# Kernel optimization log

Measured on AMD Instinct MI355X. Metric: run time of the kernel, lower is better.

The kernel has to match this reference:

```python
import jax, jax.numpy as jnp
import numpy as np

N_CHANNELS = 384  # full probe size
N_UNITS = 400     # rows of the sparse log-lik matrix
INT_SENTINEL = np.int32(2**31 - 1)


def setup_inputs() -> dict:
    key = jax.random.key(0)
    k1, k2, k3, k4, k5, k6 = jax.random.split(key, 6)
    n, r, na = 65536, 5, 32
    feats = jax.random.normal(k1, (n, r, na), dtype=jnp.float32)
    # contiguous, duplicate-free channel neighborhood per spike
    starts = jax.random.randint(k2, (n,), 0, N_CHANNELS - na)
    channels = starts[:, None] + jnp.arange(na)  # (n, na) int
    nan_mask = jax.random.uniform(k3, (n, na)) < 0.1
    feats = jnp.where(nan_mask[:, None, :], jnp.nan, feats)
    weights = jax.random.uniform(k4, (n,), dtype=jnp.float32) + 0.01
    # sparse (N_UNITS, n) log-lik matrix in COO, ~10 candidate units per spike
    nnz_per = 10
    nnz = n * nnz_per
    lik_cols = jnp.repeat(jnp.arange(n, dtype=jnp.int32), nnz_per)
    lik_rows = jax.random.randint(k5, (nnz,), 0, N_UNITS, dtype=jnp.int32)
    lik_data = jax.random.normal(k6, (nnz,), dtype=jnp.float32)
    return dict(features=feats, channels=channels, weights=weights,
                lik_rows=lik_rows, lik_cols=lik_cols, lik_data=lik_data)


def reference(features, channels, weights, lik_rows, lik_cols, lik_data):
    n, r, na = features.shape
    C = N_CHANNELS

    # --- to_full_probe: scatter sparse channel features to dense probe ---
    spike_ix = jnp.arange(n)[:, None, None]
    rank_ix = jnp.arange(r)[None, :, None]
    chan_ix = channels[:, None, :]                    # (n, 1, na) -> bcast (n, r, na)
    features_full = jnp.zeros((n, r, C), features.dtype)
    features_full = features_full.at[spike_ix, rank_ix, chan_ix].set(features)

    # finite mask on rank-0 slice, scaled by per-spike weights
    finite = jnp.isfinite(features_full[:, 0, :]).astype(features.dtype)  # (n, C)
    weights_full = finite * weights[:, None]
    features_full = jnp.nan_to_num(features_full)
    count_data = weights_full.sum(0)                  # (C,)
    weights_normalized = weights_full / count_data    # (n, C)

    # fit_mean (prior_type='none'): weighted empirical mean over spikes
    emp_mean = jnp.einsum('nc,nrc->rc', weights_normalized, features_full)  # (r, C)

    # --- sparse_reassign: per-spike-column argmax, sparse zeros = -inf ---
    offset = lik_data.min() - 1.0
    shifted = lik_data - offset                       # strictly positive
    colmax = jax.ops.segment_max(shifted, lik_cols, num_segments=n)
    is_max = shifted == colmax[lik_cols]
    cand = jnp.where(is_max, lik_rows, INT_SENTINEL)
    assign = jax.ops.segment_min(cand, lik_cols, num_segments=n)
    assignments = jnp.where(assign == INT_SENTINEL, -1, assign)  # (n,)

    return emp_mean, assignments
```

## Files before the change

kernel.cpp:

```cpp
#include <hip/hip_runtime.h>
#include <math.h>

#define NCH 384
#define RNK 5
#define NA  32
#define NSTART 384
#define NREP 8
#define CAPR 128
#define CAP (NREP*CAPR)
#define GRID 1536
#define NTILES (NSTART*4)
#define TILE_W 192
#define FLT_BIG 3.402823466e38f

#define WS_CUR   0
#define WS_TOTP  (WS_CUR + NSTART*NREP)
#define WS_MINP  (WS_TOTP + GRID)
#define WS_ORDER (WS_MINP + GRID)
#define WS_TILE  (WS_ORDER + NSTART*CAP*2)
#define WS_WORDS (WS_TILE + NTILES*TILE_W)

__device__ __forceinline__ bool finitef(float v) {
    return fabsf(v) <= FLT_BIG;
}

__global__ __launch_bounds__(256) void k_init(
    const float* __restrict__ lik_data, int nnz,
    unsigned* __restrict__ wsu, float* __restrict__ wsf)
{
    const int tid = threadIdx.x, bid = blockIdx.x;
    const int lane = tid & 63, wave = tid >> 6;
    int i = bid * 256 + tid;
    if (i < NSTART * NREP) wsu[WS_CUR + i] = 0u;

    float m = FLT_BIG;
    const int G = GRID * 256;
    const int n4 = nnz >> 2;
    const float4* d4 = (const float4*)lik_data;
    for (int j = bid * 256 + tid; j < n4; j += G) {
        float4 v = d4[j];
        m = fminf(m, fminf(fminf(v.x, v.y), fminf(v.z, v.w)));
    }
    for (int j = (n4 << 2) + bid * 256 + tid; j < nnz; j += G)
        m = fminf(m, lik_data[j]);

    #pragma unroll
    for (int o = 32; o; o >>= 1) m = fminf(m, __shfl_down(m, o));
    __shared__ float sm[4];
    if (lane == 0) sm[wave] = m;
    __syncthreads();
    if (tid == 0)
        wsf[WS_MINP + bid] = fminf(fminf(sm[0], sm[1]), fminf(sm[2], sm[3]));
}

__global__ __launch_bounds__(256) void k_prep(
    const int* __restrict__ channels, const float* __restrict__ weights,
    int n, unsigned* __restrict__ wsu, float* __restrict__ wsf)
{
    const int tid = threadIdx.x, bid = blockIdx.x;
    const int lane = tid & 63, wave = tid >> 6;
    const int rep = bid & (NREP - 1);
    const int G = GRID * 256;
    uint2* order = (uint2*)(wsu + WS_ORDER);

    float tw = 0.f;
    for (int sp = bid * 256 + tid; sp < n; sp += G) {
        const int st = channels[(size_t)sp * NA];
        const float wv = weights[sp];
        unsigned pos = atomicAdd(&wsu[WS_CUR + st * NREP + rep], 1u);
        if (pos < CAPR)
            order[(size_t)st * CAP + rep * CAPR + pos] =
                make_uint2((unsigned)sp, __float_as_uint(wv));
        tw += wv;
    }

    #pragma unroll
    for (int o = 32; o; o >>= 1) tw += __shfl_down(tw, o);
    __shared__ float st4[4];
    if (lane == 0) st4[wave] = tw;
    __syncthreads();
    if (tid == 0)
        wsf[WS_TOTP + bid] = st4[0] + st4[1] + st4[2] + st4[3];
}

__global__ __launch_bounds__(256) void k_accum(
    const float* __restrict__ feats, const unsigned* __restrict__ wsu,
    float* __restrict__ wsf)
{
    __shared__ float s_tile[TILE_W];
    const int bid = blockIdx.x, tid = threadIdx.x;
    const int b = bid >> 2, tj = bid & 3;
    const int lane = tid & 63, wave = tid >> 6;

    for (int i = tid; i < TILE_W; i += 256) s_tile[i] = 0.f;
    __syncthreads();

    float acc0 = 0.f, acc1 = 0.f, acc2 = 0.f, nanw = 0.f;
    #pragma unroll
    for (int seg = 0; seg < 2; ++seg) {
        const int rep = tj * 2 + seg;
        int cnt = (int)wsu[WS_CUR + b * NREP + rep];
        if (cnt > CAPR) cnt = CAPR;
        const uint2* order =
            (const uint2*)(wsu + WS_ORDER) + (size_t)b * CAP + rep * CAPR;
        uint2 e = make_uint2(0u, 0u);
        if (wave < cnt) e = order[wave];
        for (int k = wave; k < cnt; k += 4) {
            const int spike = (int)e.x;
            const float w = __uint_as_float(e.y);
            const float* f = feats + (size_t)spike * (RNK * NA);
            uint2 ne = make_uint2(0u, 0u);
            if (k + 4 < cnt) ne = order[k + 4];
            const float v0 = f[lane];
            const float v1 = f[lane + 64];
            const float v2 = (lane < 32) ? f[lane + 128] : 0.f;
            const float r0 = __shfl(v0, lane & 31);
            if (finitef(r0)) {
                acc0 += w * (finitef(v0) ? v0 : 0.f);
                acc1 += w * (finitef(v1) ? v1 : 0.f);
                if (lane < 32) acc2 += w * (finitef(v2) ? v2 : 0.f);
            } else if (lane < 32) {
                nanw += w;
            }
            e = ne;
        }
    }

    atomicAdd(&s_tile[lane], acc0);
    atomicAdd(&s_tile[64 + lane], acc1);
    if (lane < 32) {
        atomicAdd(&s_tile[128 + lane], acc2);
        atomicAdd(&s_tile[160 + lane], nanw);
    }
    __syncthreads();

    float* dst = wsf + WS_TILE + (size_t)bid * TILE_W;
    for (int i = tid; i < TILE_W; i += 256) dst[i] = s_tile[i];
}

__global__ __launch_bounds__(256) void k_final(
    const int* __restrict__ lik_rows, const float* __restrict__ lik_data,
    float* __restrict__ wsf, float* __restrict__ out, int n, int per)
{
    const int tid = threadIdx.x, bid = blockIdx.x;
    const int lane = tid & 63, wave = tid >> 6;
    const bool emp_block = (bid * 4 < RNK * NCH);

    float m = FLT_BIG, t = 0.f;
    if (emp_block) {
        for (int i = tid; i < GRID; i += 256) {
            m = fminf(m, wsf[WS_MINP + i]);
            t += wsf[WS_TOTP + i];
        }
    } else {
        for (int i = tid; i < GRID; i += 256)
            m = fminf(m, wsf[WS_MINP + i]);
    }
    #pragma unroll
    for (int o = 32; o; o >>= 1) {
        m = fminf(m, __shfl_down(m, o));
        t += __shfl_down(t, o);
    }
    __shared__ float sm[4], st4[4];
    if (lane == 0) { sm[wave] = m; st4[wave] = t; }
    __syncthreads();
    const float mn  = fminf(fminf(sm[0], sm[1]), fminf(sm[2], sm[3]));
    const float tot = st4[0] + st4[1] + st4[2] + st4[3];

    const float offset = mn - 1.0f;
    const int G = gridDim.x * 256;
    for (int sp = bid * 256 + tid; sp < n; sp += G) {
        const float* d  = lik_data + (size_t)sp * per;
        const int*   rr = lik_rows + (size_t)sp * per;
        float bs = -FLT_BIG;
        int br = 0x7FFFFFFF;
        for (int j = 0; j < per; ++j) {
            float s = d[j] - offset;
            int r = rr[j];
            if (s > bs) { bs = s; br = r; }
            else if (s == bs && r < br) br = r;
        }
        out[RNK * NCH + sp] = (float)br;
    }

    const int wg = bid * 4 + wave;
    if (wg < RNK * NCH) {
        const int c = wg % NCH, r = wg / NCH;
        const int db = lane & 31, half = lane >> 5;
        float s = 0.f, nb = 0.f;
        const int b = c - db;
        if (b >= 0) {
            #pragma unroll
            for (int jj = 0; jj < 2; ++jj) {
                const float* tp =
                    wsf + WS_TILE + ((size_t)b * 4 + jj * 2 + half) * TILE_W;
                s  += tp[r * 32 + db];
                nb += tp[160 + db];
            }
        }
        #pragma unroll
        for (int o = 32; o; o >>= 1) {
            s  += __shfl_down(s, o);
            nb += __shfl_down(nb, o);
        }
        if (lane == 0) out[wg] = s / (tot - nb);
    }
}

#define FB_NUM   0
#define FB_NANW  (RNK*NCH)
#define FB_TOT   (FB_NANW + NCH)
#define FB_MIN   (FB_TOT + 1)
#define FB_WORDS (FB_MIN + 1)

__device__ __forceinline__ unsigned fenc(float f) {
    unsigned u = __float_as_uint(f);
    return (u & 0x80000000u) ? ~u : (u | 0x80000000u);
}
__device__ __forceinline__ float fdec(unsigned u) {
    unsigned b = (u & 0x80000000u) ? (u ^ 0x80000000u) : ~u;
    return __uint_as_float(b);
}
__global__ void fb_init_kernel(unsigned* ws) {
    int i = blockIdx.x * blockDim.x + threadIdx.x;
    if (i < FB_WORDS) ws[i] = (i == FB_MIN) ? 0xFFFFFFFFu : 0u;
}
__global__ __launch_bounds__(256) void fb_accum_kernel(
    const float* feats, const int* channels, const float* weights,
    float* ws, int n)
{
    __shared__ float s_num[RNK * NCH];
    __shared__ float s_nanw[NCH];
    __shared__ float s_total;
    const int tid = threadIdx.x;
    for (int i = tid; i < RNK * NCH; i += 256) s_num[i] = 0.f;
    for (int i = tid; i < NCH; i += 256) s_nanw[i] = 0.f;
    if (tid == 0) s_total = 0.f;
    __syncthreads();
    const int total = n * NA;
    const int stride = gridDim.x * blockDim.x;
    float tw = 0.f;
    for (int idx = blockIdx.x * blockDim.x + tid; idx < total; idx += stride) {
        const int spike = idx >> 5, a = idx & (NA - 1);
        const int ch = channels[idx];
        const float w = weights[spike];
        if (a == 0) tw += w;
        const float* f = feats + (size_t)spike * (RNK * NA) + a;
        const float v0 = f[0];
        if (finitef(v0)) {
            atomicAdd(&s_num[ch], w * v0);
            #pragma unroll
            for (int r = 1; r < RNK; ++r) {
                float v = f[r * NA];
                if (!finitef(v)) v = 0.f;
                atomicAdd(&s_num[r * NCH + ch], w * v);
            }
        } else atomicAdd(&s_nanw[ch], w);
    }
    #pragma unroll
    for (int off = 32; off; off >>= 1) tw += __shfl_down(tw, off);
    if ((tid & 63) == 0) atomicAdd(&s_total, tw);
    __syncthreads();
    for (int i = tid; i < RNK * NCH; i += 256)
        if (s_num[i] != 0.f) atomicAdd(&ws[FB_NUM + i], s_num[i]);
    for (int i = tid; i < NCH; i += 256)
        if (s_nanw[i] != 0.f) atomicAdd(&ws[FB_NANW + i], s_nanw[i]);
    if (tid == 0) atomicAdd(&ws[FB_TOT], s_total);
}
__global__ void fb_min_kernel(const float* data, int nnz, unsigned* minw) {
    float m = FLT_BIG;
    for (int i = blockIdx.x * blockDim.x + threadIdx.x; i < nnz;
         i += gridDim.x * blockDim.x) m = fminf(m, data[i]);
    #pragma unroll
    for (int off = 32; off; off >>= 1) m = fminf(m, __shfl_down(m, off));
    if ((threadIdx.x & 63) == 0) atomicMin(minw, fenc(m));
}
__global__ void fb_finalize_kernel(const float* ws, float* out) {
    int i = blockIdx.x * blockDim.x + threadIdx.x;
    if (i < RNK * NCH) {
        int c = i % NCH;
        float cnt = ws[FB_TOT] - ws[FB_NANW + c];
        out[i] = ws[FB_NUM + i] / cnt;
    }
}
__global__ __launch_bounds__(256) void fb_assign_kernel(
    const int* rows, const float* data, const unsigned* minw,
    float* out, int n, int per)
{
    const int spike = blockIdx.x * 256 + threadIdx.x;
    if (spike >= n) return;
    const float offset = fdec(*minw) - 1.0f;
    const float* d  = data + (size_t)spike * per;
    const int*   rr = rows + (size_t)spike * per;
    float bs = -FLT_BIG;
    int br = 0x7FFFFFFF;
    for (int j = 0; j < per; ++j) {
        float s = d[j] - offset;
        int r = rr[j];
        if (s > bs) { bs = s; br = r; }
        else if (s == bs && r < br) br = r;
    }
    out[RNK * NCH + spike] = (float)br;
}

extern "C" void kernel_launch(void* const* d_in, const int* in_sizes, int n_in,
                              void* d_out, int out_size, void* d_ws, size_t ws_size,
                              hipStream_t stream) {
    const float* feats    = (const float*)d_in[0];
    const int*   channels = (const int*)d_in[1];
    const float* weights  = (const float*)d_in[2];
    const int*   lik_rows = (const int*)d_in[3];
    const float* lik_data = (const float*)d_in[5];

    int n   = in_sizes[2];
    int nnz = in_sizes[3];
    int per = nnz / n;

    float*    out = (float*)d_out;
    unsigned* wsu = (unsigned*)d_ws;
    float*    wsf = (float*)d_ws;

    const size_t req_bytes = (size_t)WS_WORDS * 4;
    const bool cap_ok = (n <= NSTART * NREP * CAPR / 4);

    if (ws_size >= req_bytes && cap_ok) {
        k_init<<<GRID, 256, 0, stream>>>(lik_data, nnz, wsu, wsf);
        k_prep<<<GRID, 256, 0, stream>>>(channels, weights, n, wsu, wsf);
        k_accum<<<NSTART * 4, 256, 0, stream>>>(feats, wsu, wsf);
        k_final<<<GRID, 256, 0, stream>>>(lik_rows, lik_data, wsf, out, n, per);
    } else {
        fb_init_kernel<<<(FB_WORDS + 255) / 256, 256, 0, stream>>>(wsu);
        fb_accum_kernel<<<1024, 256, 0, stream>>>(feats, channels, weights, wsf, n);
        fb_finalize_kernel<<<(RNK * NCH + 255) / 256, 256, 0, stream>>>(wsf, out);
        fb_min_kernel<<<256, 256, 0, stream>>>(lik_data, nnz, wsu + FB_MIN);
        fb_assign_kernel<<<(n + 255) / 256, 256, 0, stream>>>(
            lik_rows, lik_data, wsu + FB_MIN, out, n, per);
    }
}
```

Before: 42.41 us.

## Move sparse argmax assignment into accum kernel as extra blocks

The per-spike argmax reassignment moves out of the final kernel and runs in 256 extra blocks appended to the accumulation launch, so it overlaps with the feature accumulation work. The final kernel then shrinks to only the blocks needed for the empirical mean and no longer reduces the min partials. The intent is to shorten the serial tail after accumulation. In exchange, the assignment blocks now compete for compute units with the accum blocks, and the final kernel's grid size changes.

```diff
diff --git a/kernel.cpp b/kernel.cpp
--- a/kernel.cpp
+++ b/kernel.cpp
@@ -10,6 +10,8 @@
 #define CAP (NREP*CAPR)
 #define GRID 1536
 #define NTILES (NSTART*4)
+#define ASSIGN_GRID 256
+#define EMP_GRID ((RNK*NCH + 3) / 4)
 #define TILE_W 192
 #define FLT_BIG 3.402823466e38f
 
@@ -85,12 +87,44 @@
 
 __global__ __launch_bounds__(256) void k_accum(
     const float* __restrict__ feats, const unsigned* __restrict__ wsu,
-    float* __restrict__ wsf)
+    float* __restrict__ wsf,
+    const int* __restrict__ lik_rows, const float* __restrict__ lik_data,
+    float* __restrict__ out, int n, int per)
 {
     __shared__ float s_tile[TILE_W];
+    __shared__ float sm[4];
     const int bid = blockIdx.x, tid = threadIdx.x;
+    const int lane = tid & 63, wave = tid >> 6;
+
+    if (bid >= NTILES) {
+        const int abid = bid - NTILES;
+        float m = FLT_BIG;
+        for (int i = tid; i < GRID; i += 256) m = fminf(m, wsf[WS_MINP + i]);
+        #pragma unroll
+        for (int o = 32; o; o >>= 1) m = fminf(m, __shfl_down(m, o));
+        if (lane == 0) sm[wave] = m;
+        __syncthreads();
+        const float offset =
+            fminf(fminf(sm[0], sm[1]), fminf(sm[2], sm[3])) - 1.0f;
+
+        const int G = ASSIGN_GRID * 256;
+        for (int sp = abid * 256 + tid; sp < n; sp += G) {
+            const float* d  = lik_data + (size_t)sp * per;
+            const int*   rr = lik_rows + (size_t)sp * per;
+            float bs = -FLT_BIG;
+            int br = 0x7FFFFFFF;
+            for (int j = 0; j < per; ++j) {
+                float s = d[j] - offset;
+                int r = rr[j];
+                if (s > bs) { bs = s; br = r; }
+                else if (s == bs && r < br) br = r;
+            }
+            out[RNK * NCH + sp] = (float)br;
+        }
+        return;
+    }
+
     const int b = bid >> 2, tj = bid & 3;
-    const int lane = tid & 63, wave = tid >> 6;
 
     for (int i = tid; i < TILE_W; i += 256) s_tile[i] = 0.f;
     __syncthreads();
@@ -139,49 +173,19 @@
 }
 
 __global__ __launch_bounds__(256) void k_final(
-    const int* __restrict__ lik_rows, const float* __restrict__ lik_data,
-    float* __restrict__ wsf, float* __restrict__ out, int n, int per)
+    float* __restrict__ wsf, float* __restrict__ out)
 {
     const int tid = threadIdx.x, bid = blockIdx.x;
     const int lane = tid & 63, wave = tid >> 6;
-    const bool emp_block = (bid * 4 < RNK * NCH);
-
-    float m = FLT_BIG, t = 0.f;
-    if (emp_block) {
-        for (int i = tid; i < GRID; i += 256) {
-            m = fminf(m, wsf[WS_MINP + i]);
-            t += wsf[WS_TOTP + i];
-        }
-    } else {
-        for (int i = tid; i < GRID; i += 256)
-            m = fminf(m, wsf[WS_MINP + i]);
-    }
-    #pragma unroll
-    for (int o = 32; o; o >>= 1) {
-        m = fminf(m, __shfl_down(m, o));
-        t += __shfl_down(t, o);
-    }
-    __shared__ float sm[4], st4[4];
-    if (lane == 0) { sm[wave] = m; st4[wave] = t; }
-    __syncthreads();
-    const float mn  = fminf(fminf(sm[0], sm[1]), fminf(sm[2], sm[3]));
+
+    float t = 0.f;
+    for (int i = tid; i < GRID; i += 256) t += wsf[WS_TOTP + i];
+    #pragma unroll
+    for (int o = 32; o; o >>= 1) t += __shfl_down(t, o);
+    __shared__ float st4[4];
+    if (lane == 0) st4[wave] = t;
+    __syncthreads();
     const float tot = st4[0] + st4[1] + st4[2] + st4[3];
-
-    const float offset = mn - 1.0f;
-    const int G = gridDim.x * 256;
-    for (int sp = bid * 256 + tid; sp < n; sp += G) {
-        const float* d  = lik_data + (size_t)sp * per;
-        const int*   rr = lik_rows + (size_t)sp * per;
-        float bs = -FLT_BIG;
-        int br = 0x7FFFFFFF;
-        for (int j = 0; j < per; ++j) {
-            float s = d[j] - offset;
-            int r = rr[j];
-            if (s > bs) { bs = s; br = r; }
-            else if (s == bs && r < br) br = r;
-        }
-        out[RNK * NCH + sp] = (float)br;
-    }
 
     const int wg = bid * 4 + wave;
     if (wg < RNK * NCH) {
@@ -326,8 +330,9 @@
     if (ws_size >= req_bytes && cap_ok) {
         k_init<<<GRID, 256, 0, stream>>>(lik_data, nnz, wsu, wsf);
         k_prep<<<GRID, 256, 0, stream>>>(channels, weights, n, wsu, wsf);
-        k_accum<<<NSTART * 4, 256, 0, stream>>>(feats, wsu, wsf);
-        k_final<<<GRID, 256, 0, stream>>>(lik_rows, lik_data, wsf, out, n, per);
+        k_accum<<<NTILES + ASSIGN_GRID, 256, 0, stream>>>(
+            feats, wsu, wsf, lik_rows, lik_data, out, n, per);
+        k_final<<<EMP_GRID, 256, 0, stream>>>(wsf, out);
     } else {
         fb_init_kernel<<<(FB_WORDS + 255) / 256, 256, 0, stream>>>(wsu);
         fb_accum_kernel<<<1024, 256, 0, stream>>>(feats, channels, weights, wsf, n);
```

New measurement: 41.06 us. 3.2% less time.
